# Kernel tuning notes

Measured on AMD Instinct MI355X. Metric: run time of the kernel, lower is better.

Reference implementation:

```python
import jax, jax.numpy as jnp
import numpy as np

B, L, D = 4, 2048, 1024   # batch, seq_len, input_channels
S = 4096                  # param_token_num
DV = 1024                 # output_channels


def setup_inputs() -> dict:
    key = jax.random.key(0)
    k1, k2, k3 = jax.random.split(key, 3)
    return {
        "inputs": jax.random.normal(k1, (B, L, D), dtype=jnp.float32),
        "key_param_tokens": jax.random.normal(k2, (S, D), dtype=jnp.float32),
        "value_param_tokens": jax.random.normal(k3, (S, DV), dtype=jnp.float32),
    }


def reference(inputs, key_param_tokens, value_param_tokens):
    # scores: [B, L, S] — full score matrix (this is what a fused kernel would avoid)
    scores = jnp.einsum("bld,sd->bls", inputs, key_param_tokens)
    # gelu_l2_norm: exact (erf) gelu, then L2-normalize over S and rescale by sqrt(S)
    g = jax.nn.gelu(scores, approximate=False)
    l2 = jnp.linalg.norm(g, axis=-1, keepdims=True)
    w = g / l2 * jnp.sqrt(jnp.asarray(g.shape[-1], g.dtype))
    # weighted sum over param value tokens: [B, L, DV]
    return jnp.einsum("bls,sv->blv", w, value_param_tokens)
```

## Files before the change

kernel.cpp:

```cpp
#include <hip/hip_runtime.h>
#include <hip/hip_bf16.h>
#include <stdint.h>

#define M_ROWS 8192
#define D_DIM  1024
#define S_DIM  4096
#define DV_DIM 1024

typedef __attribute__((ext_vector_type(8))) short bf16x8;
typedef __attribute__((ext_vector_type(4))) float f32x4;
typedef unsigned short u16;

static __device__ __forceinline__ u16 f2bf(float x) {
  union { float f; unsigned u; } v; v.f = x;
  unsigned r = v.u + 0x7FFFu + ((v.u >> 16) & 1u);
  return (u16)(r >> 16);
}
static __device__ __forceinline__ float bf2f(u16 h) {
  union { unsigned u; float f; } v; v.u = ((unsigned)h) << 16;
  return v.f;
}
static __device__ __forceinline__ float gelu_fast(float x) {
  float u = 0.7978845608028654f * x * (1.0f + 0.044715f * x * x);
  float e = __expf(2.0f * u);
  float t = 1.0f - 2.0f / (e + 1.0f);
  return 0.5f * x * (1.0f + t);
}

static __device__ __forceinline__ void gload16(const void* g, void* l) {
  __builtin_amdgcn_global_load_lds(
      (__attribute__((address_space(1))) void*)(void*)(g),
      (__attribute__((address_space(3))) void*)(l), 16, 0, 0);
}

__global__ __launch_bounds__(256)
void cast_f32_bf16(const float* __restrict__ in, u16* __restrict__ out, int n4) {
  const int i = blockIdx.x * 256 + threadIdx.x;
  if (i >= n4) return;
  const float4 v = ((const float4*)in)[i];
  ushort4 o;
  o.x = f2bf(v.x); o.y = f2bf(v.y); o.z = f2bf(v.z); o.w = f2bf(v.w);
  ((ushort4*)out)[i] = o;
}

__global__ __launch_bounds__(256)
void transpose_cast(const float* __restrict__ V, u16* __restrict__ VT, int R, int C) {
  __shared__ float tile[32][33];
  const int tx = threadIdx.x & 31;
  const int ty = threadIdx.x >> 5;
  const int r0 = blockIdx.y * 32;
  const int c0 = blockIdx.x * 32;
#pragma unroll
  for (int dy = 0; dy < 32; dy += 8)
    tile[ty + dy][tx] = V[(long)(r0 + ty + dy) * C + (c0 + tx)];
  __syncthreads();
#pragma unroll
  for (int dy = 0; dy < 32; dy += 8)
    VT[(long)(c0 + ty + dy) * R + (r0 + tx)] = f2bf(tile[tx][ty + dy]);
}

__global__ __launch_bounds__(256)
void finalize_scale(const float* __restrict__ Pp, float* __restrict__ scale,
                    int nBN, int rows) {
  const int r = blockIdx.x * 256 + threadIdx.x;
  if (r >= rows) return;
  float s = 0.f;
  for (int j = 0; j < nBN; ++j) s += Pp[(long)r * nBN + j];
  scale[r] = 64.0f * rsqrtf(s + 1e-30f);
}


#define VMW(N) asm volatile("s_waitcnt vmcnt(" #N ")" ::: "memory")

#define PH(P, STG, WT)                                                        \
  {                                                                           \
    bf16x8 af[MF][2];                                                         \
    _Pragma("unroll")                                                         \
    for (int j = 0; j < MF; ++j) {                                            \
      const int ar = wm * MSPAN + ((P) * MF + j) * 16 + fr;                   \
      af[j][0] = rdfrag(la, ar, 0);                                           \
      af[j][1] = rdfrag(la, ar, 1);                                           \
    }                                                                         \
    STG;                                                                      \
    __builtin_amdgcn_s_barrier();                                             \
    asm volatile("s_waitcnt lgkmcnt(0)" ::: "memory");                        \
    __builtin_amdgcn_sched_barrier(0);                                        \
    __builtin_amdgcn_s_setprio(1);                                            \
    _Pragma("unroll")                                                         \
    for (int j = 0; j < MF; ++j) {                                            \
      _Pragma("unroll")                                                       \
      for (int n = 0; n < NF; ++n) {                                          \
        acc[(P) * MF + j][n] = __builtin_amdgcn_mfma_f32_16x16x32_bf16(       \
            af[j][0], bfr[n][0], acc[(P) * MF + j][n], 0, 0, 0);              \
        acc[(P) * MF + j][n] = __builtin_amdgcn_mfma_f32_16x16x32_bf16(       \
            af[j][1], bfr[n][1], acc[(P) * MF + j][n], 0, 0, 0);              \
      }                                                                       \
    }                                                                         \
    __builtin_amdgcn_s_setprio(0);                                            \
    WT;                                                                       \
    __builtin_amdgcn_s_barrier();                                             \
  }

#define READ_B                                                                \
  {                                                                           \
    _Pragma("unroll")                                                         \
    for (int n = 0; n < NF; ++n) {                                            \
      const int br = wn * NSPAN + n * 16 + fr;                                \
      bfr[n][0] = rdfrag(lb, br, 0);                                          \
      bfr[n][1] = rdfrag(lb, br, 1);                                          \
    }                                                                         \
  }

#define TILE(SAEN, SBEN, W1, W3)                                              \
  {                                                                           \
    const u16* la = ldsA[kt & 1];                                             \
    const u16* lb = ldsB[kt & 1];                                             \
    const int bA = (kt + 1) & 1;                                              \
    const int bB = kt & 1;                                                    \
    const long kA = (long)(kt + 1) * BK;                                      \
    const long kB = (long)(kt + 2) * BK;                                      \
    READ_B;                                                                   \
    if constexpr (BN == 256) {                                                \
      PH(0, if (SAEN) { SA(bA, 0, kA); SA(bA, 2, kA); }, {});                 \
      PH(1, if (SAEN) { SA(bA, 1, kA); SA(bA, 3, kA); }, W1);                 \
      PH(2, if (SBEN) { SB(bB, 0, kB); SB(bB, 1, kB); }, {});                 \
      PH(3, if (SBEN) { SB(bB, 2, kB); SB(bB, 3, kB); }, W3);                 \
    } else {                                                                  \
      PH(0, if (SAEN) { SA(bA, 0, kA); SA(bA, 1, kA); }, {});                 \
      PH(1, if (SAEN) { SA(bA, 2, kA); SA(bA, 3, kA); }, {});                 \
      PH(2, if (SBEN) { SB(bB, 0, kB); SB(bB, 1, kB); }, {});                 \
      PH(3, {}, W3);                                                          \
    }                                                                         \
  }

template <int MODE, int BN, int WM>
__global__ __launch_bounds__(512, 2)
void gemm8p(const u16* __restrict__ A, const u16* __restrict__ Bm,
            void* __restrict__ Cout, float* __restrict__ Pp,
            const float* __restrict__ scale,
            const int K, const int N, const int nBN, const int nWG) {
  constexpr int BM = 256, BK = 64;
  constexpr int WN = 8 / WM;
  constexpr int MSPAN = BM / WM;
  constexpr int NSPAN = BN / WN;
  constexpr int MF = MSPAN / 64;
  constexpr int NF = NSPAN / 16;

  __shared__ u16 ldsA[2][BM * BK];
  __shared__ u16 ldsB[2][BN * BK];

  const int tid = threadIdx.x;
  const int lane = tid & 63;
  const int wv = tid >> 6;
  const int wm = wv / WN, wn = wv % WN;
  const int fr = lane & 15, hi = lane >> 4;

  int wg;
  {
    const int q = nWG >> 3, r = nWG & 7;
    const int x = blockIdx.x & 7, ix = blockIdx.x >> 3;
    wg = (x < r ? x * (q + 1) : r * (q + 1) + (x - r) * q) + ix;
  }
  const int bm = wg / nBN, bn = wg % nBN;
  const long aR0 = (long)bm * BM;
  const long bR0 = (long)bn * BN;

  const int srow = tid >> 3;
  const int sch = (tid & 7) ^ (srow & 7);
  const long aoff = (aR0 + srow) * (long)K + sch * 8;
  const long boff = (bR0 + srow) * (long)K + sch * 8;

  auto SA = [&](int buf, int r, long kOff) {
    gload16(A + aoff + (long)r * 64 * K + kOff, &ldsA[buf][r * 4096 + tid * 8]);
  };
  auto SB = [&](int buf, int r, long kOff) {
    gload16(Bm + boff + (long)r * 64 * K + kOff, &ldsB[buf][r * 4096 + tid * 8]);
  };
  auto rdfrag = [&](const u16* base, int row, int kk) -> bf16x8 {
    return *(const bf16x8*)&base[row * 64 + (((kk << 2) | hi) ^ (row & 7)) * 8];
  };

  f32x4 acc[4 * MF][NF];
#pragma unroll
  for (int m = 0; m < 4 * MF; ++m)
#pragma unroll
    for (int n = 0; n < NF; ++n)
      acc[m][n] = f32x4{0.f, 0.f, 0.f, 0.f};

  bf16x8 bfr[NF][2];
  const int nK = K / BK;

  if constexpr (BN == 256) {
    SB(0, 0, 0); SB(0, 1, 0); SB(0, 2, 0); SB(0, 3, 0);
    SA(0, 0, 0); SA(0, 2, 0); SA(0, 1, 0); SA(0, 3, 0);
    SB(1, 0, BK); SB(1, 1, BK); SB(1, 2, BK); SB(1, 3, BK);
    VMW(6);
  } else {
    SB(0, 0, 0); SB(0, 1, 0);
    SA(0, 0, 0); SA(0, 1, 0); SA(0, 2, 0); SA(0, 3, 0);
    SB(1, 0, BK); SB(1, 1, BK);
    VMW(2);
  }
  __builtin_amdgcn_s_barrier();

  int kt = 0;
  if constexpr (BN == 256) {
    for (; kt < nK - 2; ++kt) TILE(true, true, VMW(8), VMW(6));
    TILE(true, false, VMW(8), VMW(2)); ++kt;
    TILE(false, false, VMW(0), {});
  } else {
    for (; kt < nK - 2; ++kt) TILE(true, true, {}, VMW(2));
    TILE(true, false, {}, VMW(0)); ++kt;
    TILE(false, false, {}, {});
  }

  if constexpr (MODE == 0) {
    u16* Cg = (u16*)Cout;
    float* red = (float*)&ldsA[0][0];
#pragma unroll
    for (int m = 0; m < 4 * MF; ++m) {
#pragma unroll
      for (int i = 0; i < 4; ++i) {
        const int rl = wm * MSPAN + m * 16 + hi * 4 + i;
        const long r = aR0 + rl;
        float s = 0.f;
#pragma unroll
        for (int n = 0; n < NF; ++n) {
          const float g = gelu_fast(acc[m][n][i]);
          Cg[r * N + bR0 + wn * NSPAN + n * 16 + fr] = f2bf(g);
          s += g * g;
        }
        s += __shfl_xor(s, 1); s += __shfl_xor(s, 2);
        s += __shfl_xor(s, 4); s += __shfl_xor(s, 8);
        if (fr == 0) red[rl * WN + wn] = s;
      }
    }
    __syncthreads();
    if (tid < BM) {
      float s = 0.f;
#pragma unroll
      for (int w = 0; w < WN; ++w) s += red[tid * WN + w];
      Pp[(aR0 + tid) * nBN + bn] = s;
    }
  } else {
    float* Cf = (float*)Cout;
#pragma unroll
    for (int m = 0; m < 4 * MF; ++m) {
#pragma unroll
      for (int i = 0; i < 4; ++i) {
        const long r = aR0 + wm * MSPAN + m * 16 + hi * 4 + i;
        const float s = scale[r];
#pragma unroll
        for (int n = 0; n < NF; ++n)
          Cf[r * N + bR0 + wn * NSPAN + n * 16 + fr] = acc[m][n][i] * s;
      }
    }
  }
}

extern "C" void kernel_launch(void* const* d_in, const int* in_sizes, int n_in,
                              void* d_out, int out_size, void* d_ws, size_t ws_size,
                              hipStream_t stream) {
  const float* Qf = (const float*)d_in[0];
  const float* Kf = (const float*)d_in[1];
  const float* Vf = (const float*)d_in[2];
  float* Out = (float*)d_out;

  const int M = M_ROWS, D = D_DIM, S = S_DIM, DV = DV_DIM;
  const int nBN1 = S / 256;
  const int nBN2 = DV / 128;

  char* p = (char*)d_ws;
  u16* Qb = (u16*)p;            p += (size_t)M * D * 2;
  u16* Kb = (u16*)p;            p += (size_t)S * D * 2;
  u16* VT = (u16*)p;            p += (size_t)DV * S * 2;
  float* scalebuf = (float*)p;  p += (size_t)M * 4;
  float* Pp = (float*)p;        p += (size_t)M * nBN1 * 4;
  u16* G = (u16*)p;
  const size_t fixed = (size_t)(p - (char*)d_ws);
  const size_t avail = (ws_size > fixed) ? (ws_size - fixed) : 0;

  const size_t bytes_per_row = (size_t)S * 2;
  size_t rows_fit = avail / bytes_per_row;
  int chunk = (int)((rows_fit / 256) * 256);
  if (chunk > M) chunk = M;
  if (chunk < 256) chunk = 256;

  cast_f32_bf16<<<(M * D / 4 + 255) / 256, 256, 0, stream>>>(Qf, Qb, M * D / 4);
  cast_f32_bf16<<<(S * D / 4 + 255) / 256, 256, 0, stream>>>(Kf, Kb, S * D / 4);
  transpose_cast<<<dim3(DV / 32, S / 32), 256, 0, stream>>>(Vf, VT, S, DV);

  for (int m0 = 0; m0 < M; m0 += chunk) {
    const int rows = (M - m0 < chunk) ? (M - m0) : chunk;
    const int nWG1 = (rows / 256) * nBN1;
    gemm8p<0, 256, 2><<<dim3(nWG1), 512, 0, stream>>>(
        Qb + (size_t)m0 * D, Kb, (void*)G, Pp, nullptr, D, S, nBN1, nWG1);
    finalize_scale<<<(rows + 255) / 256, 256, 0, stream>>>(Pp, scalebuf, nBN1, rows);
    const int nWG2 = (rows / 256) * nBN2;
    gemm8p<1, 128, 4><<<dim3(nWG2), 512, 0, stream>>>(
        G, VT, (void*)(Out + (size_t)m0 * DV), nullptr, scalebuf, S, DV, nBN2, nWG2);
  }
}
```

Before: 215.9 us.

## Fix 2x4 wave layout, restage GEMM prefetch schedule, drop LDS row-norm reduction

The GEMM kernel is hardcoded to a 2x4 wave grid (each wave covers 128 rows) for both GEMMs, and the K-loop prefetch order is rebuilt. Half of the next A tile is now issued in the prologue and the rest interleaved across the four phases, with different vmcnt waits. The per-row sum of squared GELU values is written straight to global memory as 64 partials per row instead of being reduced through LDS with a __syncthreads. finalize_scale reads those partials with float4 loads. The aim is better load/MFMA overlap and less epilogue sync, at the cost of more partial-sum traffic and a different wave shape for the second GEMM.

```diff
diff --git a/kernel.cpp b/kernel.cpp
--- a/kernel.cpp
+++ b/kernel.cpp
@@ -60,12 +60,16 @@
 }
 
 __global__ __launch_bounds__(256)
-void finalize_scale(const float* __restrict__ Pp, float* __restrict__ scale,
-                    int nBN, int rows) {
+void finalize_scale(const float* __restrict__ Pp, float* __restrict__ scale, int rows) {
   const int r = blockIdx.x * 256 + threadIdx.x;
   if (r >= rows) return;
+  const float4* p = (const float4*)&Pp[(long)r * 64];
   float s = 0.f;
-  for (int j = 0; j < nBN; ++j) s += Pp[(long)r * nBN + j];
+#pragma unroll
+  for (int j = 0; j < 16; ++j) {
+    const float4 v = p[j];
+    s += v.x + v.y + v.z + v.w;
+  }
   scale[r] = 64.0f * rsqrtf(s + 1e-30f);
 }
 
@@ -74,10 +78,10 @@
 
 #define PH(P, STG, WT)                                                        \
   {                                                                           \
-    bf16x8 af[MF][2];                                                         \
+    bf16x8 af[2][2];                                                          \
     _Pragma("unroll")                                                         \
-    for (int j = 0; j < MF; ++j) {                                            \
-      const int ar = wm * MSPAN + ((P) * MF + j) * 16 + fr;                   \
+    for (int j = 0; j < 2; ++j) {                                             \
+      const int ar = wm * 128 + ((P) * 2 + j) * 16 + fr;                      \
       af[j][0] = rdfrag(la, ar, 0);                                           \
       af[j][1] = rdfrag(la, ar, 1);                                           \
     }                                                                         \
@@ -87,13 +91,13 @@
     __builtin_amdgcn_sched_barrier(0);                                        \
     __builtin_amdgcn_s_setprio(1);                                            \
     _Pragma("unroll")                                                         \
-    for (int j = 0; j < MF; ++j) {                                            \
+    for (int j = 0; j < 2; ++j) {                                             \
       _Pragma("unroll")                                                       \
       for (int n = 0; n < NF; ++n) {                                          \
-        acc[(P) * MF + j][n] = __builtin_amdgcn_mfma_f32_16x16x32_bf16(       \
-            af[j][0], bfr[n][0], acc[(P) * MF + j][n], 0, 0, 0);              \
-        acc[(P) * MF + j][n] = __builtin_amdgcn_mfma_f32_16x16x32_bf16(       \
-            af[j][1], bfr[n][1], acc[(P) * MF + j][n], 0, 0, 0);              \
+        acc[(P) * 2 + j][n] = __builtin_amdgcn_mfma_f32_16x16x32_bf16(        \
+            af[j][0], bfr[n][0], acc[(P) * 2 + j][n], 0, 0, 0);               \
+        acc[(P) * 2 + j][n] = __builtin_amdgcn_mfma_f32_16x16x32_bf16(        \
+            af[j][1], bfr[n][1], acc[(P) * 2 + j][n], 0, 0, 0);               \
       }                                                                       \
     }                                                                         \
     __builtin_amdgcn_s_setprio(0);                                            \
@@ -111,39 +115,14 @@
     }                                                                         \
   }
 
-#define TILE(SAEN, SBEN, W1, W3)                                              \
-  {                                                                           \
-    const u16* la = ldsA[kt & 1];                                             \
-    const u16* lb = ldsB[kt & 1];                                             \
-    const int bA = (kt + 1) & 1;                                              \
-    const int bB = kt & 1;                                                    \
-    const long kA = (long)(kt + 1) * BK;                                      \
-    const long kB = (long)(kt + 2) * BK;                                      \
-    READ_B;                                                                   \
-    if constexpr (BN == 256) {                                                \
-      PH(0, if (SAEN) { SA(bA, 0, kA); SA(bA, 2, kA); }, {});                 \
-      PH(1, if (SAEN) { SA(bA, 1, kA); SA(bA, 3, kA); }, W1);                 \
-      PH(2, if (SBEN) { SB(bB, 0, kB); SB(bB, 1, kB); }, {});                 \
-      PH(3, if (SBEN) { SB(bB, 2, kB); SB(bB, 3, kB); }, W3);                 \
-    } else {                                                                  \
-      PH(0, if (SAEN) { SA(bA, 0, kA); SA(bA, 1, kA); }, {});                 \
-      PH(1, if (SAEN) { SA(bA, 2, kA); SA(bA, 3, kA); }, {});                 \
-      PH(2, if (SBEN) { SB(bB, 0, kB); SB(bB, 1, kB); }, {});                 \
-      PH(3, {}, W3);                                                          \
-    }                                                                         \
-  }
-
-template <int MODE, int BN, int WM>
+template <int MODE, int BN>
 __global__ __launch_bounds__(512, 2)
 void gemm8p(const u16* __restrict__ A, const u16* __restrict__ Bm,
             void* __restrict__ Cout, float* __restrict__ Pp,
             const float* __restrict__ scale,
             const int K, const int N, const int nBN, const int nWG) {
   constexpr int BM = 256, BK = 64;
-  constexpr int WN = 8 / WM;
-  constexpr int MSPAN = BM / WM;
-  constexpr int NSPAN = BN / WN;
-  constexpr int MF = MSPAN / 64;
+  constexpr int NSPAN = BN / 4;
   constexpr int NF = NSPAN / 16;
 
   __shared__ u16 ldsA[2][BM * BK];
@@ -152,7 +131,7 @@
   const int tid = threadIdx.x;
   const int lane = tid & 63;
   const int wv = tid >> 6;
-  const int wm = wv / WN, wn = wv % WN;
+  const int wm = wv >> 2, wn = wv & 3;
   const int fr = lane & 15, hi = lane >> 4;
 
   int wg;
@@ -180,9 +159,9 @@
     return *(const bf16x8*)&base[row * 64 + (((kk << 2) | hi) ^ (row & 7)) * 8];
   };
 
-  f32x4 acc[4 * MF][NF];
-#pragma unroll
-  for (int m = 0; m < 4 * MF; ++m)
+  f32x4 acc[8][NF];
+#pragma unroll
+  for (int m = 0; m < 8; ++m)
 #pragma unroll
     for (int n = 0; n < NF; ++n)
       acc[m][n] = f32x4{0.f, 0.f, 0.f, 0.f};
@@ -192,37 +171,70 @@
 
   if constexpr (BN == 256) {
     SB(0, 0, 0); SB(0, 1, 0); SB(0, 2, 0); SB(0, 3, 0);
-    SA(0, 0, 0); SA(0, 2, 0); SA(0, 1, 0); SA(0, 3, 0);
+    SA(0, 0, 0); SA(0, 1, 0); SA(0, 2, 0); SA(0, 3, 0);
     SB(1, 0, BK); SB(1, 1, BK); SB(1, 2, BK); SB(1, 3, BK);
+    SA(1, 0, BK); SA(1, 2, BK);
     VMW(6);
   } else {
     SB(0, 0, 0); SB(0, 1, 0);
     SA(0, 0, 0); SA(0, 1, 0); SA(0, 2, 0); SA(0, 3, 0);
     SB(1, 0, BK); SB(1, 1, BK);
-    VMW(2);
+    SA(1, 0, BK); SA(1, 2, BK);
+    VMW(4);
   }
   __builtin_amdgcn_s_barrier();
 
-  int kt = 0;
-  if constexpr (BN == 256) {
-    for (; kt < nK - 2; ++kt) TILE(true, true, VMW(8), VMW(6));
-    TILE(true, false, VMW(8), VMW(2)); ++kt;
-    TILE(false, false, VMW(0), {});
-  } else {
-    for (; kt < nK - 2; ++kt) TILE(true, true, {}, VMW(2));
-    TILE(true, false, {}, VMW(0)); ++kt;
-    TILE(false, false, {}, {});
+  for (int kt = 0; kt < nK - 2; ++kt) {
+    const u16* la = ldsA[kt & 1];
+    const u16* lb = ldsB[kt & 1];
+    const int bO = (kt + 1) & 1;
+    const int bS = kt & 1;
+    const long kA1 = (long)(kt + 1) * BK;
+    const long kA2 = (long)(kt + 2) * BK;
+    READ_B;
+    if constexpr (BN == 256) {
+      PH(0, { SA(bO, 1, kA1); SA(bO, 3, kA1); }, {});
+      PH(1, { SB(bS, 0, kA2); SB(bS, 1, kA2); }, {});
+      PH(2, { SB(bS, 2, kA2); SB(bS, 3, kA2); }, {});
+      PH(3, { SA(bS, 0, kA2); SA(bS, 2, kA2); }, VMW(6));
+    } else {
+      PH(0, { SA(bO, 1, kA1); SA(bO, 3, kA1); }, {});
+      PH(1, { SB(bS, 0, kA2); SB(bS, 1, kA2); }, {});
+      PH(2, { SA(bS, 0, kA2); SA(bS, 2, kA2); }, {});
+      PH(3, {}, VMW(4));
+    }
+  }
+
+  {
+    const int kt = nK - 2;
+    const u16* la = ldsA[kt & 1];
+    const u16* lb = ldsB[kt & 1];
+    const int bO = (kt + 1) & 1;
+    const long kA1 = (long)(kt + 1) * BK;
+    READ_B;
+    PH(0, { SA(bO, 1, kA1); SA(bO, 3, kA1); }, {});
+    PH(1, {}, {});
+    PH(2, {}, {});
+    PH(3, {}, VMW(0));
+  }
+  {
+    const int kt = nK - 1;
+    const u16* la = ldsA[kt & 1];
+    const u16* lb = ldsB[kt & 1];
+    READ_B;
+    PH(0, {}, {});
+    PH(1, {}, {});
+    PH(2, {}, {});
+    PH(3, {}, {});
   }
 
   if constexpr (MODE == 0) {
     u16* Cg = (u16*)Cout;
-    float* red = (float*)&ldsA[0][0];
-#pragma unroll
-    for (int m = 0; m < 4 * MF; ++m) {
+#pragma unroll
+    for (int m = 0; m < 8; ++m) {
 #pragma unroll
       for (int i = 0; i < 4; ++i) {
-        const int rl = wm * MSPAN + m * 16 + hi * 4 + i;
-        const long r = aR0 + rl;
+        const long r = aR0 + wm * 128 + m * 16 + hi * 4 + i;
         float s = 0.f;
 #pragma unroll
         for (int n = 0; n < NF; ++n) {
@@ -232,23 +244,16 @@
         }
         s += __shfl_xor(s, 1); s += __shfl_xor(s, 2);
         s += __shfl_xor(s, 4); s += __shfl_xor(s, 8);
-        if (fr == 0) red[rl * WN + wn] = s;
+        if (fr == 0) Pp[r * 64 + bn * 4 + wn] = s;
       }
-    }
-    __syncthreads();
-    if (tid < BM) {
-      float s = 0.f;
-#pragma unroll
-      for (int w = 0; w < WN; ++w) s += red[tid * WN + w];
-      Pp[(aR0 + tid) * nBN + bn] = s;
     }
   } else {
     float* Cf = (float*)Cout;
 #pragma unroll
-    for (int m = 0; m < 4 * MF; ++m) {
+    for (int m = 0; m < 8; ++m) {
 #pragma unroll
       for (int i = 0; i < 4; ++i) {
-        const long r = aR0 + wm * MSPAN + m * 16 + hi * 4 + i;
+        const long r = aR0 + wm * 128 + m * 16 + hi * 4 + i;
         const float s = scale[r];
 #pragma unroll
         for (int n = 0; n < NF; ++n)
@@ -275,7 +280,7 @@
   u16* Kb = (u16*)p;            p += (size_t)S * D * 2;
   u16* VT = (u16*)p;            p += (size_t)DV * S * 2;
   float* scalebuf = (float*)p;  p += (size_t)M * 4;
-  float* Pp = (float*)p;        p += (size_t)M * nBN1 * 4;
+  float* Pp = (float*)p;        p += (size_t)M * 64 * 4;
   u16* G = (u16*)p;
   const size_t fixed = (size_t)(p - (char*)d_ws);
   const size_t avail = (ws_size > fixed) ? (ws_size - fixed) : 0;
@@ -293,11 +298,11 @@
   for (int m0 = 0; m0 < M; m0 += chunk) {
     const int rows = (M - m0 < chunk) ? (M - m0) : chunk;
     const int nWG1 = (rows / 256) * nBN1;
-    gemm8p<0, 256, 2><<<dim3(nWG1), 512, 0, stream>>>(
+    gemm8p<0, 256><<<dim3(nWG1), 512, 0, stream>>>(
         Qb + (size_t)m0 * D, Kb, (void*)G, Pp, nullptr, D, S, nBN1, nWG1);
-    finalize_scale<<<(rows + 255) / 256, 256, 0, stream>>>(Pp, scalebuf, nBN1, rows);
+    finalize_scale<<<(rows + 255) / 256, 256, 0, stream>>>(Pp, scalebuf, rows);
     const int nWG2 = (rows / 256) * nBN2;
-    gemm8p<1, 128, 4><<<dim3(nWG2), 512, 0, stream>>>(
+    gemm8p<1, 128><<<dim3(nWG2), 512, 0, stream>>>(
         G, VT, (void*)(Out + (size_t)m0 * DV), nullptr, scalebuf, S, DV, nBN2, nWG2);
   }
 }
```

Result: slower. 220.3 us (+2.0%).
